# Optimization experiments

Measured on AMD Instinct MI355X. Metric: run time of the kernel, lower is better.

## Reference

```python
import jax, jax.numpy as jnp
import numpy as np

N_NODES = 50000
N_EDGES = 1000000
HID = 64
L = 3
EPS_MSG = 1e-7   # GENConv message eps
EPS_SM = 1e-16   # PyG scatter-softmax denominator eps
LN_EPS = 1e-5


def layernorm(x, g, b):
    mu = jnp.mean(x, axis=-1, keepdims=True)
    var = jnp.var(x, axis=-1, keepdims=True)
    return (x - mu) * jax.lax.rsqrt(var + LN_EPS) * g + b


def genconv(x, src, dst, edge_attr, t, W1, b1, g1, be1, W2, b2):
    # message: relu(x_j + e_ij) + eps  -> [E, HID]
    msg = jax.nn.relu(x[src] + edge_attr) + EPS_MSG
    # softmax aggregation over incoming edges of each dst node
    logits = msg * t
    m = jax.ops.segment_max(logits, dst, num_segments=N_NODES)
    m = jnp.where(jnp.isfinite(m), m, 0.0)
    e = jnp.exp(logits - m[dst])
    s = jax.ops.segment_sum(e, dst, num_segments=N_NODES) + EPS_SM
    agg = jax.ops.segment_sum((e / s[dst]) * msg, dst, num_segments=N_NODES)
    # root residual + MLP [64 -> 128 -> 64]
    h = agg + x
    h = h @ W1 + b1
    h = jax.nn.relu(layernorm(h, g1, be1))
    return h @ W2 + b2


def setup_inputs() -> dict:
    key = jax.random.key(0)
    ks = jax.random.split(key, 10)
    inp = {
        'x': jax.random.normal(ks[0], (N_NODES, 16), jnp.float32),
        'edge_attr': jax.random.uniform(ks[1], (N_EDGES, 1), jnp.float32),
        'edge_index': jax.random.randint(ks[2], (2, N_EDGES), 0, N_NODES, jnp.int32),
        'W_node': jax.random.normal(ks[3], (16, HID), jnp.float32) / np.sqrt(16.0),
        'b_node': jnp.zeros((HID,), jnp.float32),
        'W_edge': jax.random.normal(ks[4], (1, HID), jnp.float32),
        'b_edge': jnp.zeros((HID,), jnp.float32),
        't': jnp.ones((L,), jnp.float32),
        'W1': jax.random.normal(ks[5], (L, HID, 2 * HID), jnp.float32) / np.sqrt(float(HID)),
        'b1': jnp.zeros((L, 2 * HID), jnp.float32),
        'ln_g': jnp.ones((L, 2 * HID), jnp.float32),
        'ln_b': jnp.zeros((L, 2 * HID), jnp.float32),
        'W2': jax.random.normal(ks[6], (L, 2 * HID, HID), jnp.float32) / np.sqrt(2.0 * HID),
        'b2': jnp.zeros((L, HID), jnp.float32),
        'norm_g': jnp.ones((L, HID), jnp.float32),
        'norm_b': jnp.zeros((L, HID), jnp.float32),
        'W_lin': jax.random.normal(ks[7], (HID, 64), jnp.float32) / np.sqrt(float(HID)),
        'b_lin': jnp.zeros((64,), jnp.float32),
    }
    return inp


def reference(x, edge_attr, edge_index, W_node, b_node, W_edge, b_edge, t,
              W1, b1, ln_g, ln_b, W2, b2, norm_g, norm_b, W_lin, b_lin):
    src, dst = edge_index[0], edge_index[1]
    h = x @ W_node + b_node                 # [N, HID]
    ea = edge_attr @ W_edge + b_edge        # [E, HID]
    # layer 0: conv only
    h = genconv(h, src, dst, ea, t[0], W1[0], b1[0], ln_g[0], ln_b[0], W2[0], b2[0])
    # layers 1..L-1: res+ blocks (norm -> relu -> conv -> residual); dropout is identity in eval
    for i in range(1, L):
        z = jax.nn.relu(layernorm(h, norm_g[i], norm_b[i]))
        h = h + genconv(z, src, dst, ea, t[i], W1[i], b1[i], ln_g[i], ln_b[i], W2[i], b2[i])
    # final norm/act reuses layer 0's norm
    h = jax.nn.relu(layernorm(h, norm_g[0], norm_b[0]))
    # adaptive avg/max pool (N, 64) -> (1, 32): pool over all nodes, channel bins of 2
    avg = h.mean(axis=0).reshape(32, 2).mean(axis=1)
    mx = h.max(axis=0).reshape(32, 2).max(axis=1)
    emb = jnp.concatenate([avg, mx])[None, :]   # [1, 64]
    return emb @ W_lin + b_lin                  # [1, 64]
```

## Files before the change

kernel.cpp:

```cpp
#include <hip/hip_runtime.h>
#include <math.h>

#define N_NODES 50000
#define N_EDGES 1000000
#define HID 64
#define CAP 64
#define N_TILES (N_NODES / 16)
#define NB_MLP 782
#define VB_S 72
#define UB_S 136
#define NB_ENC ((N_NODES + 3) / 4)
#define NB_WPREP ((3 * 8192 + 255) / 256)
#define NBK 196
#define BKCAP 6144
#define EPB 4096
#define NB1 ((N_EDGES + EPB - 1) / EPB)
static_assert(N_NODES % 16 == 0, "tile math");
static_assert(N_NODES <= 65536, "src must fit in 16 bits");

typedef __attribute__((ext_vector_type(8))) short short8;
typedef __attribute__((ext_vector_type(4))) float f32x4;

__device__ __forceinline__ unsigned short f2bf(float x) {
    unsigned u = __float_as_uint(x);
    u += 0x7FFFu + ((u >> 16) & 1u);
    return (unsigned short)(u >> 16);
}
__device__ __forceinline__ float bfbits_hi(unsigned pk) {
    return __uint_as_float(pk & 0xFFFF0000u);
}
__device__ __forceinline__ float bf2f(unsigned short v) {
    return __uint_as_float(((unsigned)v) << 16);
}
__device__ __forceinline__ unsigned addpk(unsigned a, unsigned b) {
    float lo = __uint_as_float(a << 16) + __uint_as_float(b << 16);
    float hi = __uint_as_float(a & 0xFFFF0000u) + __uint_as_float(b & 0xFFFF0000u);
    return (unsigned)f2bf(lo) | ((unsigned)f2bf(hi) << 16);
}

__global__ __launch_bounds__(256) void k_front(
    const float* __restrict__ x, const float* __restrict__ Wn,
    const float* __restrict__ bn, unsigned short* __restrict__ zb,
    const float* __restrict__ W1, const float* __restrict__ W2,
    unsigned short* __restrict__ w1p, unsigned short* __restrict__ w2p,
    const int* __restrict__ ei, const float* __restrict__ eattr,
    int* __restrict__ gcnt, uint2* __restrict__ coarse) {
    __shared__ unsigned pk_l[EPB];
    __shared__ unsigned short dst_l[EPB];
    __shared__ unsigned spk[EPB];
    __shared__ unsigned short sdst[EPB];
    __shared__ int hist[NBK], loc[NBK], gbase[NBK], cur[NBK];
    __shared__ int inc[256];
    int b = blockIdx.x;
    if (b < NB1) {
        int tid = threadIdx.x;
        int e0 = b * EPB;
        int nel = N_EDGES - e0; if (nel > EPB) nel = EPB;
        for (int q = tid; q < NBK; q += 256) { hist[q] = 0; cur[q] = 0; }
        __syncthreads();
        for (int j = tid; j < nel; j += 256) {
            int i = e0 + j;
            int d = ei[N_EDGES + i];
            unsigned pk = ((unsigned)f2bf(eattr[i]) << 16) | (unsigned)(ei[i] & 0xFFFF);
            pk_l[j] = pk; dst_l[j] = (unsigned short)d;
            atomicAdd(&hist[d >> 8], 1);
        }
        __syncthreads();
        int v = (tid < NBK) ? hist[tid] : 0;
        inc[tid] = v;
        __syncthreads();
        #pragma unroll
        for (int dd = 1; dd < 256; dd <<= 1) {
            int t2 = (tid >= dd) ? inc[tid - dd] : 0;
            __syncthreads();
            inc[tid] += t2;
            __syncthreads();
        }
        if (tid < NBK) {
            loc[tid] = inc[tid] - v;
            gbase[tid] = atomicAdd(&gcnt[tid], v);
        }
        __syncthreads();
        for (int j = tid; j < nel; j += 256) {
            int bkt = dst_l[j] >> 8;
            int r = atomicAdd(&cur[bkt], 1);
            int pos = loc[bkt] + r;
            spk[pos] = pk_l[j]; sdst[pos] = dst_l[j];
        }
        __syncthreads();
        for (int j = tid; j < nel; j += 256) {
            int d = sdst[j];
            int bkt = d >> 8;
            int off = gbase[bkt] + (j - loc[bkt]);
            if (off < BKCAP) coarse[(size_t)bkt * BKCAP + off] = make_uint2(spk[j], (unsigned)d);
        }
    } else if (b < NB1 + NB_ENC) {
        int n = (b - NB1) * 4 + (threadIdx.x >> 6);
        int c = threadIdx.x & 63;
        if (n >= N_NODES) return;
        float acc = bn[c];
        const float* xr = x + n * 16;
        #pragma unroll
        for (int k = 0; k < 16; ++k) acc = fmaf(xr[k], Wn[k * 64 + c], acc);
        zb[n * 64 + c] = f2bf(acc);
    } else {
        int i = (b - NB1 - NB_ENC) * 256 + threadIdx.x;
        if (i >= 3 * 8192) return;
        int L = i >> 13, r = i & 8191;
        int j = r & 7, lane = (r >> 3) & 63;
        int quad = lane >> 4, col = lane & 15;
        {
            int st = r >> 9;
            int s = st >> 3, t = st & 7;
            w1p[i] = f2bf(W1[L * 8192 + (s * 32 + quad * 8 + j) * 128 + t * 16 + col]);
        }
        {
            int ft = r >> 9;
            int s = ft >> 2, t = ft & 3;
            w2p[i] = f2bf(W2[L * 8192 + (s * 32 + quad * 8 + j) * 64 + t * 16 + col]);
        }
    }
}

__global__ __launch_bounds__(256) void k_bin2(
    const int* __restrict__ gcnt, const uint2* __restrict__ coarse,
    int* __restrict__ cnt, unsigned int* __restrict__ s_pack) {
    __shared__ unsigned epk[BKCAP];
    __shared__ unsigned char eln[BKCAP];
    __shared__ unsigned spk[BKCAP];
    __shared__ unsigned char sln[BKCAP];
    __shared__ int hist[256], cur[256], inc2[256];
    int tid = threadIdx.x;
    int b = blockIdx.x;
    int m = gcnt[b]; if (m > BKCAP) m = BKCAP;
    hist[tid] = 0; cur[tid] = 0;
    __syncthreads();
    for (int j = tid; j < m; j += 256) {
        uint2 e = coarse[(size_t)b * BKCAP + j];
        epk[j] = e.x;
        int ln = (int)(e.y & 255u);
        eln[j] = (unsigned char)ln;
        atomicAdd(&hist[ln], 1);
    }
    __syncthreads();
    int v = hist[tid];
    inc2[tid] = v;
    __syncthreads();
    #pragma unroll
    for (int dd = 1; dd < 256; dd <<= 1) {
        int t2 = (tid >= dd) ? inc2[tid - dd] : 0;
        __syncthreads();
        inc2[tid] += t2;
        __syncthreads();
    }
    int lv = inc2[tid] - v;
    __syncthreads();
    hist[tid] = lv;
    int node = b * 256 + tid;
    if (node < N_NODES) cnt[node] = v;
    __syncthreads();
    for (int j = tid; j < m; j += 256) {
        int ln = eln[j];
        int r = atomicAdd(&cur[ln], 1);
        int pos = hist[ln] + r;
        spk[pos] = epk[j]; sln[pos] = (unsigned char)ln;
    }
    __syncthreads();
    for (int j = tid; j < m; j += 256) {
        int ln = sln[j];
        int k = j - hist[ln];
        if (k < CAP) s_pack[(size_t)(b * 256 + ln) * CAP + k] = spk[j];
    }
}

__global__ __launch_bounds__(256) void k_agg(
    const unsigned short* __restrict__ zb, const int* __restrict__ cnt,
    const unsigned int* __restrict__ s_pack,
    const float* __restrict__ We, const float* __restrict__ be,
    const float* __restrict__ t, int layer, unsigned short* __restrict__ aggb) {
    int wid = (blockIdx.x * blockDim.x + threadIdx.x) >> 6;
    int lane = threadIdx.x & 63;
    if (wid >= N_NODES) return;
    int deg = cnt[wid];
    deg = (deg < CAP) ? deg : CAP;
    int beg = wid * CAP, end = beg + deg;
    int half = lane >> 5;
    int c2 = lane & 31;
    float we0 = We[2 * c2], we1 = We[2 * c2 + 1];
    float bv0 = be[2 * c2], bv1 = be[2 * c2 + 1];
    float tl = t[layer];
    const unsigned* zbu = (const unsigned*)zb;
    float s0 = 0.f, s1 = 0.f, n0 = 0.f, n1 = 0.f;
    int i = beg;
    for (; i + 15 < end; i += 16) {
        unsigned pk[8];
        #pragma unroll
        for (int j = 0; j < 8; ++j) {
            unsigned pa = s_pack[i + 2 * j];
            unsigned pb = s_pack[i + 2 * j + 1];
            pk[j] = half ? pb : pa;
        }
        unsigned zu[8];
        #pragma unroll
        for (int j = 0; j < 8; ++j) zu[j] = zbu[(pk[j] & 0xFFFFu) * 32 + c2];
        #pragma unroll
        for (int j = 0; j < 8; ++j) {
            float ea = bfbits_hi(pk[j]);
            float z0 = __uint_as_float(zu[j] << 16);
            float z1 = __uint_as_float(zu[j] & 0xFFFF0000u);
            float m0 = fmaxf(z0 + fmaf(ea, we0, bv0), 0.f) + 1e-7f;
            float m1 = fmaxf(z1 + fmaf(ea, we1, bv1), 0.f) + 1e-7f;
            float p0 = __expf(m0 * tl), p1 = __expf(m1 * tl);
            s0 += p0; n0 = fmaf(p0, m0, n0);
            s1 += p1; n1 = fmaf(p1, m1, n1);
        }
    }
    for (; i + 7 < end; i += 8) {
        unsigned pk[4];
        #pragma unroll
        for (int j = 0; j < 4; ++j) {
            unsigned pa = s_pack[i + 2 * j];
            unsigned pb = s_pack[i + 2 * j + 1];
            pk[j] = half ? pb : pa;
        }
        unsigned zu[4];
        #pragma unroll
        for (int j = 0; j < 4; ++j) zu[j] = zbu[(pk[j] & 0xFFFFu) * 32 + c2];
        #pragma unroll
        for (int j = 0; j < 4; ++j) {
            float ea = bfbits_hi(pk[j]);
            float z0 = __uint_as_float(zu[j] << 16);
            float z1 = __uint_as_float(zu[j] & 0xFFFF0000u);
            float m0 = fmaxf(z0 + fmaf(ea, we0, bv0), 0.f) + 1e-7f;
            float m1 = fmaxf(z1 + fmaf(ea, we1, bv1), 0.f) + 1e-7f;
            float p0 = __expf(m0 * tl), p1 = __expf(m1 * tl);
            s0 += p0; n0 = fmaf(p0, m0, n0);
            s1 += p1; n1 = fmaf(p1, m1, n1);
        }
    }
    for (; i + 1 < end; i += 2) {
        unsigned pa = s_pack[i], pb = s_pack[i + 1];
        unsigned pk = half ? pb : pa;
        unsigned zu = zbu[(pk & 0xFFFFu) * 32 + c2];
        float ea = bfbits_hi(pk);
        float z0 = __uint_as_float(zu << 16);
        float z1 = __uint_as_float(zu & 0xFFFF0000u);
        float m0 = fmaxf(z0 + fmaf(ea, we0, bv0), 0.f) + 1e-7f;
        float m1 = fmaxf(z1 + fmaf(ea, we1, bv1), 0.f) + 1e-7f;
        float p0 = __expf(m0 * tl), p1 = __expf(m1 * tl);
        s0 += p0; n0 = fmaf(p0, m0, n0);
        s1 += p1; n1 = fmaf(p1, m1, n1);
    }
    if (i < end) {
        unsigned pk = s_pack[i];
        unsigned zu = zbu[(pk & 0xFFFFu) * 32 + c2];
        float ea = bfbits_hi(pk);
        float z0 = __uint_as_float(zu << 16);
        float z1 = __uint_as_float(zu & 0xFFFF0000u);
        float m0 = fmaxf(z0 + fmaf(ea, we0, bv0), 0.f) + 1e-7f;
        float m1 = fmaxf(z1 + fmaf(ea, we1, bv1), 0.f) + 1e-7f;
        float p0 = __expf(m0 * tl), p1 = __expf(m1 * tl);
        if (half == 0) {
            s0 += p0; n0 = fmaf(p0, m0, n0);
            s1 += p1; n1 = fmaf(p1, m1, n1);
        }
    }
    s0 += __shfl_xor(s0, 32, 64); n0 += __shfl_xor(n0, 32, 64);
    s1 += __shfl_xor(s1, 32, 64); n1 += __shfl_xor(n1, 32, 64);
    if (half == 0) {
        unsigned r = (unsigned)f2bf(n0 / (s0 + 1e-16f)) |
                     ((unsigned)f2bf(n1 / (s1 + 1e-16f)) << 16);
        ((unsigned*)aggb)[wid * 32 + c2] = r;
    }
}

__global__ __launch_bounds__(256) void k_mlp(
    const unsigned short* __restrict__ aggb, unsigned short* __restrict__ zb,
    unsigned short* __restrict__ hb,
    const unsigned short* __restrict__ w1p, const unsigned short* __restrict__ w2p,
    const float* __restrict__ b1,
    const float* __restrict__ g1, const float* __restrict__ be1,
    const float* __restrict__ b2,
    const float* __restrict__ ng, const float* __restrict__ nb, int mode,
    float* __restrict__ pb_sum, float* __restrict__ pb_max) {
    __shared__ unsigned short w1s[8192];
    __shared__ unsigned short w2s[8192];
    __shared__ unsigned short vbuf[4][16 * VB_S];
    __shared__ unsigned short ubuf[4][16 * UB_S];
    __shared__ float lssum[4][4][16], lsmax[4][4][16];
    int lane = threadIdx.x & 63;
    int wave = threadIdx.x >> 6;
    int col = lane & 15, quad = lane >> 4;
    unsigned short* vb = vbuf[wave];
    unsigned short* ub = ubuf[wave];

    {
        const uint4* s1 = (const uint4*)w1p;
        const uint4* s2 = (const uint4*)w2p;
        uint4* d1 = (uint4*)w1s;
        uint4* d2 = (uint4*)w2s;
        #pragma unroll
        for (int i = 0; i < 4; ++i) {
            d1[threadIdx.x + i * 256] = s1[threadIdx.x + i * 256];
            d2[threadIdx.x + i * 256] = s2[threadIdx.x + i * 256];
        }
    }
    __syncthreads();

    float b1f[8], g1f[8], e1f[8];
    #pragma unroll
    for (int t = 0; t < 8; ++t) {
        int ch = t * 16 + col;
        b1f[t] = b1[ch]; g1f[t] = g1[ch]; e1f[t] = be1[ch];
    }
    float b2f_[4], ngf[4], nbf[4];
    #pragma unroll
    for (int t = 0; t < 4; ++t) {
        b2f_[t] = b2[t * 16 + col];
        ngf[t] = ng[t * 16 + col];
        nbf[t] = nb[t * 16 + col];
    }

    float psum[4] = {0.f, 0.f, 0.f, 0.f};
    float pmax[4] = {0.f, 0.f, 0.f, 0.f};
    int nd = lane >> 2;
    int cg = (lane & 3) * 16;

    for (int tile = blockIdx.x * 4 + wave; tile < N_TILES; tile += NB_MLP * 4) {
        int n0 = tile * 16;
        const uint4* ap = (const uint4*)(aggb + (size_t)(n0 + nd) * 64 + cg);
        const uint4* zp = (const uint4*)(zb + (size_t)(n0 + nd) * 64 + cg);
        uint4 a0 = ap[0], a1 = ap[1], z0 = zp[0], z1 = zp[1];
        uint4 r0, r1;
        r0.x = addpk(a0.x, z0.x); r0.y = addpk(a0.y, z0.y);
        r0.z = addpk(a0.z, z0.z); r0.w = addpk(a0.w, z0.w);
        r1.x = addpk(a1.x, z1.x); r1.y = addpk(a1.y, z1.y);
        r1.z = addpk(a1.z, z1.z); r1.w = addpk(a1.w, z1.w);
        uint4* vdst = (uint4*)&vb[nd * VB_S + cg];
        vdst[0] = r0;
        vdst[1] = r1;

        short8 af0 = *(const short8*)&vb[col * VB_S + quad * 8];
        short8 af1 = *(const short8*)&vb[col * VB_S + 32 + quad * 8];

        uint4 h0, h1;
        if (mode >= 1) {
            const uint4* hp = (const uint4*)(hb + (size_t)(n0 + nd) * 64 + cg);
            h0 = hp[0]; h1 = hp[1];
        }

        f32x4 au[8];
        #pragma unroll
        for (int t = 0; t < 8; ++t) {
            short8 w0 = *(const short8*)&w1s[((0 * 8 + t) * 64 + lane) * 8];
            short8 w1 = *(const short8*)&w1s[((1 * 8 + t) * 64 + lane) * 8];
            f32x4 c = {0.f, 0.f, 0.f, 0.f};
            c = __builtin_amdgcn_mfma_f32_16x16x32_bf16(af0, w0, c, 0, 0, 0);
            c = __builtin_amdgcn_mfma_f32_16x16x32_bf16(af1, w1, c, 0, 0, 0);
            au[t] = c;
        }
        #pragma unroll
        for (int r = 0; r < 4; ++r) {
            float sx = 0.f, sq = 0.f;
            #pragma unroll
            for (int t = 0; t < 8; ++t) {
                float v = au[t][r] + b1f[t];
                sx += v; sq += v * v;
            }
            #pragma unroll
            for (int mask = 1; mask < 16; mask <<= 1) {
                sx += __shfl_xor(sx, mask, 64);
                sq += __shfl_xor(sq, mask, 64);
            }
            float mu = sx * (1.f / 128.f);
            float var = sq * (1.f / 128.f) - mu * mu;
            float rs = rsqrtf(var + 1e-5f);
            int row = quad * 4 + r;
            #pragma unroll
            for (int t = 0; t < 8; ++t) {
                float v = au[t][r] + b1f[t];
                float y = fmaxf(fmaf((v - mu) * rs, g1f[t], e1f[t]), 0.f);
                ub[row * UB_S + t * 16 + col] = f2bf(y);
            }
        }
        f32x4 oc[4];
        #pragma unroll
        for (int t = 0; t < 4; ++t) oc[t] = (f32x4){0.f, 0.f, 0.f, 0.f};
        #pragma unroll
        for (int s = 0; s < 4; ++s) {
            short8 a = *(const short8*)&ub[col * UB_S + s * 32 + quad * 8];
            #pragma unroll
            for (int t = 0; t < 4; ++t) {
                short8 w = *(const short8*)&w2s[((s * 4 + t) * 64 + lane) * 8];
                oc[t] = __builtin_amdgcn_mfma_f32_16x16x32_bf16(a, w, oc[t], 0, 0, 0);
            }
        }
        if (mode >= 1) {
            uint4* hdst = (uint4*)&vb[nd * VB_S + cg];
            hdst[0] = h0;
            hdst[1] = h1;
        }
        #pragma unroll
        for (int r = 0; r < 4; ++r) {
            int row = quad * 4 + r;
            float val[4];
            #pragma unroll
            for (int t = 0; t < 4; ++t) {
                val[t] = oc[t][r] + b2f_[t];
                if (mode >= 1) val[t] += bf2f(vb[row * VB_S + t * 16 + col]);
            }
            float sx = 0.f, sq = 0.f;
            #pragma unroll
            for (int t = 0; t < 4; ++t) { sx += val[t]; sq += val[t] * val[t]; }
            #pragma unroll
            for (int mask = 1; mask < 16; mask <<= 1) {
                sx += __shfl_xor(sx, mask, 64);
                sq += __shfl_xor(sq, mask, 64);
            }
            float mu = sx * (1.f / 64.f);
            float var = sq * (1.f / 64.f) - mu * mu;
            float rs = rsqrtf(var + 1e-5f);
            #pragma unroll
            for (int t = 0; t < 4; ++t) {
                float y = fmaxf(fmaf((val[t] - mu) * rs, ngf[t], nbf[t]), 0.f);
                if (mode <= 1) {
                    vb[row * VB_S + t * 16 + col] = f2bf(val[t]);
                    ub[row * UB_S + t * 16 + col] = f2bf(y);
                } else {
                    psum[t] += y;
                    pmax[t] = fmaxf(pmax[t], y);
                }
            }
        }
        if (mode <= 1) {
            const uint4* hsrc = (const uint4*)&vb[nd * VB_S + cg];
            const uint4* zsrc = (const uint4*)&ub[nd * UB_S + cg];
            uint4* hdst = (uint4*)(hb + (size_t)(n0 + nd) * 64 + cg);
            uint4* zdst = (uint4*)(zb + (size_t)(n0 + nd) * 64 + cg);
            hdst[0] = hsrc[0]; hdst[1] = hsrc[1];
            zdst[0] = zsrc[0]; zdst[1] = zsrc[1];
        }
    }
    if (mode == 2) {
        #pragma unroll
        for (int t = 0; t < 4; ++t) {
            psum[t] += __shfl_xor(psum[t], 16, 64);
            psum[t] += __shfl_xor(psum[t], 32, 64);
            pmax[t] = fmaxf(pmax[t], __shfl_xor(pmax[t], 16, 64));
            pmax[t] = fmaxf(pmax[t], __shfl_xor(pmax[t], 32, 64));
        }
        if (quad == 0) {
            #pragma unroll
            for (int t = 0; t < 4; ++t) {
                lssum[wave][t][col] = psum[t];
                lsmax[wave][t][col] = pmax[t];
            }
        }
        __syncthreads();
        if (wave == 0) {
            int t = lane >> 4, c = lane & 15;
            float s = lssum[0][t][c] + lssum[1][t][c] + lssum[2][t][c] + lssum[3][t][c];
            float mx = fmaxf(fmaxf(lsmax[0][t][c], lsmax[1][t][c]),
                             fmaxf(lsmax[2][t][c], lsmax[3][t][c]));
            pb_sum[blockIdx.x * 64 + lane] = s;
            pb_max[blockIdx.x * 64 + lane] = mx;
        }
    }
}

__global__ __launch_bounds__(1024) void k_head(
    const float* __restrict__ pb_sum, const float* __restrict__ pb_max,
    const float* __restrict__ Wl, const float* __restrict__ bl, float* __restrict__ out) {
    __shared__ float sa4[16][64], sm4[16][64];
    __shared__ float sa[64], sm[64], emb[64];
    int t = threadIdx.x;
    int ch = t & 63, part = t >> 6;
    float s = 0.f, mx = 0.f;
    for (int b = part; b < NB_MLP; b += 16) {
        s += pb_sum[b * 64 + ch];
        mx = fmaxf(mx, pb_max[b * 64 + ch]);
    }
    sa4[part][ch] = s; sm4[part][ch] = mx;
    __syncthreads();
    if (t < 64) {
        float ss = 0.f, mm = 0.f;
        #pragma unroll
        for (int q = 0; q < 16; ++q) {
            ss += sa4[q][t];
            mm = fmaxf(mm, sm4[q][t]);
        }
        sa[t] = ss; sm[t] = mm;
    }
    __syncthreads();
    if (t < 64) {
        if (t < 32) {
            emb[t] = (sa[2 * t] + sa[2 * t + 1]) * (0.5f / (float)N_NODES);
        } else {
            int i = t - 32;
            emb[t] = fmaxf(sm[2 * i], sm[2 * i + 1]);
        }
    }
    __syncthreads();
    if (t < 64) {
        float acc = bl[t];
        for (int k = 0; k < 64; ++k) acc = fmaf(emb[k], Wl[k * 64 + t], acc);
        out[t] = acc;
    }
}

extern "C" void kernel_launch(void* const* d_in, const int* in_sizes, int n_in,
                              void* d_out, int out_size, void* d_ws, size_t ws_size,
                              hipStream_t stream) {
    const float* x     = (const float*)d_in[0];
    const float* eattr = (const float*)d_in[1];
    const int*   ei    = (const int*)d_in[2];
    const float* Wn    = (const float*)d_in[3];
    const float* bn    = (const float*)d_in[4];
    const float* We    = (const float*)d_in[5];
    const float* be    = (const float*)d_in[6];
    const float* t     = (const float*)d_in[7];
    const float* W1    = (const float*)d_in[8];
    const float* b1    = (const float*)d_in[9];
    const float* lg    = (const float*)d_in[10];
    const float* lb    = (const float*)d_in[11];
    const float* W2    = (const float*)d_in[12];
    const float* b2    = (const float*)d_in[13];
    const float* ng    = (const float*)d_in[14];
    const float* nb    = (const float*)d_in[15];
    const float* Wl    = (const float*)d_in[16];
    const float* bl    = (const float*)d_in[17];
    float* out = (float*)d_out;

    char* p = (char*)d_ws;
    unsigned short* hb   = (unsigned short*)p; p += (size_t)N_NODES * 64 * 2;
    unsigned short* zb   = (unsigned short*)p; p += (size_t)N_NODES * 64 * 2;
    unsigned short* aggb = (unsigned short*)p; p += (size_t)N_NODES * 64 * 2;
    unsigned int* s_pack = (unsigned int*)p; p += (size_t)N_NODES * CAP * 4;
    int* cnt    = (int*)p;  p += (size_t)N_NODES * 4;
    int* gcnt   = (int*)p;  p += (size_t)256 * 4;
    uint2* coarse = (uint2*)p; p += (size_t)NBK * BKCAP * 8;
    float* pb_sum = (float*)p; p += (size_t)NB_MLP * 64 * 4;
    float* pb_max = (float*)p; p += (size_t)NB_MLP * 64 * 4;
    unsigned short* w1p = (unsigned short*)p; p += (size_t)3 * 8192 * 2;
    unsigned short* w2p = (unsigned short*)p; p += (size_t)3 * 8192 * 2;

    hipMemsetAsync(gcnt, 0, (size_t)NBK * sizeof(int), stream);

    k_front<<<NB1 + NB_ENC + NB_WPREP, 256, 0, stream>>>(
        x, Wn, bn, zb, W1, W2, w1p, w2p, ei, eattr, gcnt, coarse);
    k_bin2<<<NBK, 256, 0, stream>>>(gcnt, coarse, cnt, s_pack);

    k_agg<<<(N_NODES + 3) / 4, 256, 0, stream>>>(zb, cnt, s_pack, We, be, t, 0, aggb);
    k_mlp<<<NB_MLP, 256, 0, stream>>>(aggb, zb, hb, w1p, w2p, b1, lg, lb, b2,
                                      ng + 64, nb + 64, 0, pb_sum, pb_max);
    k_agg<<<(N_NODES + 3) / 4, 256, 0, stream>>>(zb, cnt, s_pack, We, be, t, 1, aggb);
    k_mlp<<<NB_MLP, 256, 0, stream>>>(aggb, zb, hb, w1p + 8192, w2p + 8192,
                                      b1 + 128, lg + 128, lb + 128, b2 + 64,
                                      ng + 128, nb + 128, 1, pb_sum, pb_max);
    k_agg<<<(N_NODES + 3) / 4, 256, 0, stream>>>(zb, cnt, s_pack, We, be, t, 2, aggb);
    k_mlp<<<NB_MLP, 256, 0, stream>>>(aggb, zb, hb, w1p + 2 * 8192, w2p + 2 * 8192,
                                      b1 + 2 * 128, lg + 2 * 128, lb + 2 * 128, b2 + 2 * 64,
                                      ng, nb, 2, pb_sum, pb_max);

    k_head<<<1, 1024, 0, stream>>>(pb_sum, pb_max, Wl, bl, out);
}
```

Before: 299.3 us.

## Split each bin2 bucket across two blocks and sort edges by source per node

k_bin2 now launches two blocks per coarse bucket, with each block handling half of the 256 destination nodes. This doubles the number of blocks, but each block still reads the whole bucket. After the per-node scatter, the edges of each node are insertion-sorted by source index, with one thread per node. Sorting is meant to improve gather locality of zb rows in the three later k_agg passes. The sort is serial per thread and adds shared-memory work for high-degree nodes.

After: 358.2 us. 19.7% more time.

```diff
diff --git a/kernel.cpp b/kernel.cpp
--- a/kernel.cpp
+++ b/kernel.cpp
@@ -129,47 +129,65 @@
     __shared__ unsigned char eln[BKCAP];
     __shared__ unsigned spk[BKCAP];
     __shared__ unsigned char sln[BKCAP];
-    __shared__ int hist[256], cur[256], inc2[256];
+    __shared__ int hist[128], loc[128], cur[128], inc2[128];
     int tid = threadIdx.x;
-    int b = blockIdx.x;
-    int m = gcnt[b]; if (m > BKCAP) m = BKCAP;
-    hist[tid] = 0; cur[tid] = 0;
+    int bkt = blockIdx.x >> 1;
+    int hsel = blockIdx.x & 1;
+    int m = gcnt[bkt]; if (m > BKCAP) m = BKCAP;
+    if (tid < 128) { hist[tid] = 0; cur[tid] = 0; }
     __syncthreads();
     for (int j = tid; j < m; j += 256) {
-        uint2 e = coarse[(size_t)b * BKCAP + j];
+        uint2 e = coarse[(size_t)bkt * BKCAP + j];
         epk[j] = e.x;
         int ln = (int)(e.y & 255u);
         eln[j] = (unsigned char)ln;
-        atomicAdd(&hist[ln], 1);
-    }
-    __syncthreads();
-    int v = hist[tid];
-    inc2[tid] = v;
+        if ((ln >> 7) == hsel) atomicAdd(&hist[ln & 127], 1);
+    }
+    __syncthreads();
+    int v = (tid < 128) ? hist[tid] : 0;
+    if (tid < 128) inc2[tid] = v;
     __syncthreads();
     #pragma unroll
-    for (int dd = 1; dd < 256; dd <<= 1) {
-        int t2 = (tid >= dd) ? inc2[tid - dd] : 0;
-        __syncthreads();
-        inc2[tid] += t2;
-        __syncthreads();
-    }
-    int lv = inc2[tid] - v;
-    __syncthreads();
-    hist[tid] = lv;
-    int node = b * 256 + tid;
-    if (node < N_NODES) cnt[node] = v;
-    __syncthreads();
+    for (int dd = 1; dd < 128; dd <<= 1) {
+        int t2 = (tid >= dd && tid < 128) ? inc2[tid - dd] : 0;
+        __syncthreads();
+        if (tid < 128) inc2[tid] += t2;
+        __syncthreads();
+    }
+    if (tid < 128) {
+        loc[tid] = inc2[tid] - v;
+        int node = bkt * 256 + hsel * 128 + tid;
+        if (node < N_NODES) cnt[node] = v;
+    }
+    __syncthreads();
+    int mh = inc2[127];
     for (int j = tid; j < m; j += 256) {
         int ln = eln[j];
-        int r = atomicAdd(&cur[ln], 1);
-        int pos = hist[ln] + r;
-        spk[pos] = epk[j]; sln[pos] = (unsigned char)ln;
-    }
-    __syncthreads();
-    for (int j = tid; j < m; j += 256) {
+        if ((ln >> 7) == hsel) {
+            int r = atomicAdd(&cur[ln & 127], 1);
+            int pos = loc[ln & 127] + r;
+            spk[pos] = epk[j]; sln[pos] = (unsigned char)ln;
+        }
+    }
+    __syncthreads();
+    if (tid < 128 && v > 1) {
+        int b0 = loc[tid];
+        for (int a = b0 + 1; a < b0 + v; ++a) {
+            unsigned key = spk[a];
+            int kb = (int)(key & 0xFFFFu);
+            int c = a - 1;
+            while (c >= b0 && (int)(spk[c] & 0xFFFFu) > kb) {
+                spk[c + 1] = spk[c];
+                --c;
+            }
+            spk[c + 1] = key;
+        }
+    }
+    __syncthreads();
+    for (int j = tid; j < mh; j += 256) {
         int ln = sln[j];
-        int k = j - hist[ln];
-        if (k < CAP) s_pack[(size_t)(b * 256 + ln) * CAP + k] = spk[j];
+        int k = j - loc[ln & 127];
+        if (k < CAP) s_pack[(size_t)(bkt * 256 + ln) * CAP + k] = spk[j];
     }
 }
 
@@ -532,8 +550,8 @@
     float* out = (float*)d_out;
 
     char* p = (char*)d_ws;
-    unsigned short* hb   = (unsigned short*)p; p += (size_t)N_NODES * 64 * 2;
-    unsigned short* zb   = (unsigned short*)p; p += (size_t)N_NODES * 64 * 2;
+    unsigned short* hb = (unsigned short*)p; p += (size_t)N_NODES * 64 * 2;
+    unsigned short* zb = (unsigned short*)p; p += (size_t)N_NODES * 64 * 2;
     unsigned short* aggb = (unsigned short*)p; p += (size_t)N_NODES * 64 * 2;
     unsigned int* s_pack = (unsigned int*)p; p += (size_t)N_NODES * CAP * 4;
     int* cnt    = (int*)p;  p += (size_t)N_NODES * 4;
@@ -548,7 +566,7 @@
 
     k_front<<<NB1 + NB_ENC + NB_WPREP, 256, 0, stream>>>(
         x, Wn, bn, zb, W1, W2, w1p, w2p, ei, eattr, gcnt, coarse);
-    k_bin2<<<NBK, 256, 0, stream>>>(gcnt, coarse, cnt, s_pack);
+    k_bin2<<<NBK * 2, 256, 0, stream>>>(gcnt, coarse, cnt, s_pack);
 
     k_agg<<<(N_NODES + 3) / 4, 256, 0, stream>>>(zb, cnt, s_pack, We, be, t, 0, aggb);
     k_mlp<<<NB_MLP, 256, 0, stream>>>(aggb, zb, hb, w1p, w2p, b1, lg, lb, b2,
```
